# Kernel optimization log

Measured on AMD Instinct MI355X. Metric: run time of the kernel, lower is better.

Reference implementation:

```python
import jax, jax.numpy as jnp
import numpy as np

B, T, D, K = 64, 4096, 90, 32
LOG2PI = 1.8378770664093453


def setup_inputs() -> dict:
    key = jax.random.key(0)
    k1, k2, k3, k4, k5 = jax.random.split(key, 5)
    X = jax.random.normal(k1, (B, T, D), dtype=jnp.float32)
    state_priors = jax.random.uniform(k2, (K,), dtype=jnp.float32)
    transition_matrix = jax.random.uniform(k3, (K, K), dtype=jnp.float32)
    mu = jax.random.normal(k4, (K, D), dtype=jnp.float32) * 0.5
    log_var = jax.random.normal(k5, (K, D), dtype=jnp.float32) * 0.1
    return {"X": X, "state_priors": state_priors,
            "transition_matrix": transition_matrix, "mu": mu, "log_var": log_var}


def _emission_logprobs(X, mu, log_var):
    # Diagonal-Gaussian log density per state: (B,T,K)
    # expand (x-mu)^2*inv_var to avoid materializing a (B,T,K,D) tensor
    inv_var = jnp.exp(-log_var)                                   # (K,D)
    quad = (jnp.einsum('btd,kd->btk', X * X, inv_var)
            - 2.0 * jnp.einsum('btd,kd->btk', X, mu * inv_var)
            + jnp.sum(mu * mu * inv_var, axis=-1))                # (B,T,K)
    return -0.5 * (quad + jnp.sum(log_var, axis=-1) + D * LOG2PI)


def reference(X, state_priors, transition_matrix, mu, log_var):
    log_A = jax.nn.log_softmax(transition_matrix, axis=1)   # (K,K)
    log_pi = jax.nn.log_softmax(state_priors, axis=0)       # (K,)
    em = _emission_logprobs(X, mu, log_var)                 # (B,T,K)

    log_alpha0 = log_pi + em[:, 0, :]                       # (B,K)

    def step(log_alpha, e_t):
        # log_alpha: (B,K), e_t: (B,K)
        la = e_t + jax.nn.logsumexp(log_alpha[:, :, None] + log_A[None], axis=1)
        return la, None

    em_rest = jnp.swapaxes(em[:, 1:, :], 0, 1)              # (T-1,B,K)
    log_alpha_T, _ = jax.lax.scan(step, log_alpha0, em_rest)
    # sum over subjects of logsumexp over states at final timestep
    return jnp.sum(jax.nn.logsumexp(log_alpha_T, axis=-1))
```

## Files before the change

### kernel.cpp

```cpp
#include <hip/hip_runtime.h>
#include <stdint.h>

#define B_ 64
#define T_ 4096
#define D_ 90
#define K_ 32
#define CH_ 32
#define F_  128

typedef float f32x16 __attribute__((ext_vector_type(16)));
typedef __bf16 bf16x8 __attribute__((ext_vector_type(8)));

#define WS_A     0
#define WS_PI    1024
#define WS_C0    1056
#define WS_WF    1088
#define WS_EACC  4160
#define WS_MS    12352
#define WS_E     20544
#define WS_Q     4214848

__device__ __forceinline__ int perm_r(int r) {
  int t2 = (r >> 2) & 3;
  return r + ((t2 == 1) ? 4 : (t2 == 2) ? -4 : 0);
}
__device__ __forceinline__ uint32_t pk2(float hi, float lo) {
  return __builtin_amdgcn_perm(__float_as_uint(hi), __float_as_uint(lo), 0x07060302u);
}
__device__ __forceinline__ uint32_t rnd_pk(float hi, float lo) {
  uint32_t uh = __float_as_uint(hi) + 0x8000u;
  uint32_t ul = __float_as_uint(lo) + 0x8000u;
  return __builtin_amdgcn_perm(uh, ul, 0x07060302u);
}
__device__ __forceinline__ float bf2f(ushort u) {
  return __uint_as_float(((uint32_t)u) << 16);
}
__device__ __forceinline__ bf16x8 mkbf(uint32_t a, uint32_t b, uint32_t c, uint32_t d) {
  union { uint32_t u[4]; bf16x8 v; } x;
  x.u[0] = a; x.u[1] = b; x.u[2] = c; x.u[3] = d;
  return x.v;
}

__global__ __launch_bounds__(1024) void prep_kernel(
    const float* __restrict__ priors, const float* __restrict__ trans,
    const float* __restrict__ mu, const float* __restrict__ lv,
    float* __restrict__ ws) {
  int tid = threadIdx.x;
  {
    float v = trans[tid];
    float m = v;
    #pragma unroll
    for (int mk = 16; mk; mk >>= 1) m = fmaxf(m, __shfl_xor(m, mk));
    float e = expf(v - m);
    float s = e;
    #pragma unroll
    for (int mk = 16; mk; mk >>= 1) s += __shfl_xor(s, mk);
    ws[WS_A + tid] = e / s;
  }
  if (tid < 32) {
    float v = priors[tid];
    float m = v;
    #pragma unroll
    for (int mk = 16; mk; mk >>= 1) m = fmaxf(m, __shfl_xor(m, mk));
    float e = expf(v - m);
    float s = e;
    #pragma unroll
    for (int mk = 16; mk; mk >>= 1) s += __shfl_xor(s, mk);
    ws[WS_PI + tid] = e / s;
  }
  for (int i = tid; i < 6144; i += 1024) {
    int j = i & 7, l = (i >> 3) & 63, cm = i >> 9;
    int c = cm >> 1, mat = cm & 1;
    int h = l >> 5, nn = l & 31;
    int d = 16 * c + 8 * h + j;
    float v = 0.0f;
    if (d < D_) {
      float ivd = expf(-lv[nn * D_ + d]);
      v = (mat == 0) ? -0.5f * ivd : mu[nn * D_ + d] * ivd;
    }
    ((ushort*)(ws + WS_WF))[i] = (ushort)((__float_as_uint(v) + 0x8000u) >> 16);
  }
  if (tid < 32) {
    float s = 0.0f;
    for (int d = 0; d < D_; ++d) {
      float l  = lv[tid * D_ + d];
      float iv = expf(-l);
      float m_ = mu[tid * D_ + d];
      s += m_ * m_ * iv + l;
    }
    ws[WS_C0 + tid] = -0.5f * (s + (float)D_ * 1.8378770664093453f);
  }
}

__global__ __launch_bounds__(256) void emis_kernel(const float* __restrict__ X,
                                                   float* __restrict__ ws) {
  __shared__ float xs[4 * 2888];
  int tid = threadIdx.x;
  int l = tid & 63;
  int w = tid >> 6;
  int n = l & 31, h = l >> 5;
  int tB = blockIdx.x << 7;
  const float4* Xg = (const float4*)(X + (size_t)tB * D_);
  #pragma unroll
  for (int it = 0; it < 12; ++it) {
    int i = tid + (it << 8);
    if (i < 2880) {
      int g = i / 720;
      ((float4*)xs)[g * 722 + (i - g * 720)] = Xg[i];
    }
  }
  const uint4* wfp = (const uint4*)((const ushort*)(ws + WS_WF));
  uint4 wf[12];
  #pragma unroll
  for (int cm = 0; cm < 12; ++cm) wf[cm] = wfp[cm * 64 + l];
  float c0 = ws[WS_C0 + n];
  __syncthreads();
  int t0 = tB + (w << 5);
  int b  = t0 >> 12;
  const float* xrow = xs + w * 2888 + n * 90;
  f32x16 acc1, acc2;
  #pragma unroll
  for (int r = 0; r < 16; ++r) { acc1[r] = 0.0f; acc2[r] = 0.0f; }
  #pragma unroll
  for (int c = 0; c < 6; ++c) {
    float x[8];
    int s = 16 * c + 8 * h;
    const float2* p = (const float2*)(xrow + s);
    #pragma unroll
    for (int r = 0; r < 4; ++r) { float2 v = p[r]; x[2*r] = v.x; x[2*r+1] = v.y; }
    if (c == 5) {
      #pragma unroll
      for (int j = 0; j < 8; ++j) if (s + j >= D_) x[j] = 0.0f;
    }
    union { uint32_t u[4]; bf16x8 v; } xb, x2b;
    #pragma unroll
    for (int r = 0; r < 4; ++r) {
      xb.u[r]  = rnd_pk(x[2*r+1], x[2*r]);
      x2b.u[r] = rnd_pk(x[2*r+1] * x[2*r+1], x[2*r] * x[2*r]);
    }
    union { uint4 u; bf16x8 v; } w2, w1;
    w2.u = wf[c * 2]; w1.u = wf[c * 2 + 1];
    acc1 = __builtin_amdgcn_mfma_f32_32x32x16_bf16(xb.v,  w1.v, acc1, 0, 0, 0);
    acc2 = __builtin_amdgcn_mfma_f32_32x32x16_bf16(x2b.v, w2.v, acc2, 0, 0, 0);
  }
  float em[16], mrow[16];
  #pragma unroll
  for (int r = 0; r < 16; ++r) {
    float v = acc1[r] + acc2[r] + c0;
    em[r] = v;
    float m = v;
    #pragma unroll
    for (int mk = 1; mk <= 16; mk <<= 1) m = fmaxf(m, __shfl_xor(m, mk));
    mrow[r] = m;
  }
  ushort* Ew = (ushort*)(ws + WS_E);
  size_t ebase = (size_t)(b * K_ + n) * T_ + (t0 & (T_ - 1));
  #pragma unroll
  for (int q = 0; q < 4; ++q) {
    float e0 = exp2f((em[4*q]   - mrow[4*q])   * 1.44269504088896f);
    float e1 = exp2f((em[4*q+1] - mrow[4*q+1]) * 1.44269504088896f);
    float e2 = exp2f((em[4*q+2] - mrow[4*q+2]) * 1.44269504088896f);
    float e3 = exp2f((em[4*q+3] - mrow[4*q+3]) * 1.44269504088896f);
    uint2 d;
    d.x = rnd_pk(e1, e0);
    d.y = rnd_pk(e3, e2);
    *(uint2*)(Ew + ebase + 8 * q + 4 * h) = d;
  }
  float msum = 0.0f;
  #pragma unroll
  for (int r = 0; r < 16; ++r) msum += mrow[r];
  msum += __shfl_xor(msum, 32);
  if (l == 0) ws[WS_MS + (t0 >> 5)] = msum;
}

__global__ __launch_bounds__(128) void chunk_kernel(float* __restrict__ ws) {
  int l = threadIdx.x & 63;
  int h = l >> 5, n = l & 31;
  int bc = (blockIdx.x << 1) | (threadIdx.x >> 6);
  int b = bc >> 7, c = bc & (F_ - 1);
  int col = perm_r(n);
  const float* A = ws + WS_A;
  float astat[16];
  #pragma unroll
  for (int j = 0; j < 8; ++j) {
    astat[j]     = A[(8 * h + j) * K_ + col];
    astat[8 + j] = A[(16 + 8 * h + j) * K_ + col];
  }
  uint32_t q[8];
  #pragma unroll
  for (int r = 0; r < 4; ++r) {
    int s0 = 8 * h + 2 * r;
    uint32_t lo = (s0 == n)     ? 0x3F80u : 0u;
    uint32_t hi = (s0 + 1 == n) ? 0x3F80u : 0u;
    q[r] = lo | (hi << 16);
    int s2 = s0 + 16;
    lo = (s2 == n)     ? 0x3F80u : 0u;
    hi = (s2 + 1 == n) ? 0x3F80u : 0u;
    q[4 + r] = lo | (hi << 16);
  }
  const ushort* Eb = (const ushort*)(ws + WS_E) + (size_t)(b * K_ + col) * T_ + c * CH_;
  int eacc = 0;
  const f32x16 z = {0.f,0.f,0.f,0.f,0.f,0.f,0.f,0.f,0.f,0.f,0.f,0.f,0.f,0.f,0.f,0.f};
  f32x16 acc;
  #pragma unroll
  for (int r = 0; r < 16; ++r) acc[r] = 0.0f;

  auto step = [&](float e0) {
    uint32_t au[8];
    #pragma unroll
    for (int r = 0; r < 4; ++r) {
      au[r]     = pk2(astat[2 * r + 1] * e0, astat[2 * r] * e0);
      au[4 + r] = pk2(astat[8 + 2 * r + 1] * e0, astat[8 + 2 * r] * e0);
    }
    bf16x8 alo = mkbf(au[0], au[1], au[2], au[3]);
    bf16x8 ahi = mkbf(au[4], au[5], au[6], au[7]);
    bf16x8 qlo = mkbf(q[0], q[1], q[2], q[3]);
    bf16x8 qhi = mkbf(q[4], q[5], q[6], q[7]);
    acc = __builtin_amdgcn_mfma_f32_32x32x16_bf16(alo, qlo, z, 0, 0, 0);
    acc = __builtin_amdgcn_mfma_f32_32x32x16_bf16(ahi, qhi, acc, 0, 0, 0);
    #pragma unroll
    for (int r = 0; r < 4; ++r) {
      q[r]     = pk2(acc[2 * r + 1], acc[2 * r]);
      q[4 + r] = pk2(acc[8 + 2 * r + 1], acc[8 + 2 * r]);
    }
  };
  auto renorm = [&]() {
    float m = acc[0];
    #pragma unroll
    for (int r = 1; r < 16; ++r) m = fmaxf(m, acc[r]);
    #pragma unroll
    for (int mk = 1; mk <= 32; mk <<= 1) m = fmaxf(m, __shfl_xor(m, mk));
    int ex;
    frexpf(m, &ex);
    float sc = ldexpf(1.0f, -ex);
    eacc += ex;
    #pragma unroll
    for (int r = 0; r < 16; ++r) acc[r] *= sc;
    #pragma unroll
    for (int r = 0; r < 4; ++r) {
      q[r]     = pk2(acc[2 * r + 1], acc[2 * r]);
      q[4 + r] = pk2(acc[8 + 2 * r + 1], acc[8 + 2 * r]);
    }
  };

  uint4 ev = *(const uint4*)(Eb);
  int gstart = 0;
  if (c == 0) {
    uint4 evn = *(const uint4*)(Eb + 8);
    #pragma unroll
    for (int j = 1; j < 8; ++j) {
      uint32_t u = ((const uint32_t*)&ev)[j >> 1];
      step(bf2f((j & 1) ? (ushort)(u >> 16) : (ushort)(u & 0xFFFF)));
    }
    renorm();
    ev = evn;
    gstart = 1;
  }
  for (int g = gstart; g < CH_ / 8; ++g) {
    uint4 evn;
    if (g < CH_ / 8 - 1) evn = *(const uint4*)(Eb + 8 * (g + 1));
    #pragma unroll
    for (int j = 0; j < 8; ++j) {
      uint32_t u = ((const uint32_t*)&ev)[j >> 1];
      step(bf2f((j & 1) ? (ushort)(u >> 16) : (ushort)(u & 0xFFFF)));
    }
    renorm();
    ev = evn;
  }
  float* Qout = ws + WS_Q + (size_t)bc * (K_ * K_);
  #pragma unroll
  for (int r = 0; r < 16; ++r) {
    int m_ = (r & 3) + 8 * (r >> 2) + 4 * h;
    Qout[perm_r(m_) * K_ + n] = acc[r];
  }
  if (l == 0) ((int*)ws)[WS_EACC + bc] = eacc;
}

__global__ __launch_bounds__(512) void combine_kernel(float* __restrict__ ws,
                                                      float* __restrict__ out) {
  __shared__ float pm[8][32 * 34];
  __shared__ int   pe[8];
  int tid = threadIdx.x;
  int l = tid & 63, w = tid >> 6;
  int h = l >> 5, n = l & 31;
  int b = blockIdx.x;
  int row = perm_r(n);
  const float* Qb = ws + WS_Q + (size_t)b * (F_ * K_ * K_);
  const ushort* Ew = (const ushort*)(ws + WS_E);
  float alpha0 = 0.0f, msm = 0.0f;
  if (w == 0) {
    alpha0 = ws[WS_PI + n] * bf2f(Ew[(size_t)(b * K_ + n) * T_]);
    msm = ws[WS_MS + b * 128 + l] + ws[WS_MS + b * 128 + 64 + l];
  }
  int eacc = 0;
  {
    const int* ea = ((const int*)ws) + WS_EACC + b * F_ + w * 16;
    int v = (l < 16) ? ea[l] : 0;
    #pragma unroll
    for (int mk = 1; mk <= 8; mk <<= 1) v += __shfl_xor(v, mk);
    eacc = __shfl(v, 0);
  }
  uint32_t q[8];
  #pragma unroll
  for (int r = 0; r < 4; ++r) {
    int s0 = 8 * h + 2 * r;
    uint32_t lo = (s0 == n)     ? 0x3F80u : 0u;
    uint32_t hi = (s0 + 1 == n) ? 0x3F80u : 0u;
    q[r] = lo | (hi << 16);
    int s2 = s0 + 16;
    lo = (s2 == n)     ? 0x3F80u : 0u;
    hi = (s2 + 1 == n) ? 0x3F80u : 0u;
    q[4 + r] = lo | (hi << 16);
  }
  f32x16 acc;
  #pragma unroll
  for (int r = 0; r < 16; ++r) acc[r] = 0.0f;
  const f32x16 z = {0.f,0.f,0.f,0.f,0.f,0.f,0.f,0.f,0.f,0.f,0.f,0.f,0.f,0.f,0.f,0.f};

  auto lmul = [&](const float* a) {
    uint32_t au[8];
    #pragma unroll
    for (int r = 0; r < 4; ++r) {
      au[r]     = pk2(a[2 * r + 1], a[2 * r]);
      au[4 + r] = pk2(a[8 + 2 * r + 1], a[8 + 2 * r]);
    }
    bf16x8 alo = mkbf(au[0], au[1], au[2], au[3]);
    bf16x8 ahi = mkbf(au[4], au[5], au[6], au[7]);
    bf16x8 qlo = mkbf(q[0], q[1], q[2], q[3]);
    bf16x8 qhi = mkbf(q[4], q[5], q[6], q[7]);
    acc = __builtin_amdgcn_mfma_f32_32x32x16_bf16(alo, qlo, z, 0, 0, 0);
    acc = __builtin_amdgcn_mfma_f32_32x32x16_bf16(ahi, qhi, acc, 0, 0, 0);
    #pragma unroll
    for (int r = 0; r < 4; ++r) {
      q[r]     = pk2(acc[2 * r + 1], acc[2 * r]);
      q[4 + r] = pk2(acc[8 + 2 * r + 1], acc[8 + 2 * r]);
    }
  };
  auto renorm = [&]() {
    float m = acc[0];
    #pragma unroll
    for (int r = 1; r < 16; ++r) m = fmaxf(m, acc[r]);
    #pragma unroll
    for (int mk = 1; mk <= 32; mk <<= 1) m = fmaxf(m, __shfl_xor(m, mk));
    int ex;
    frexpf(m, &ex);
    float sc = ldexpf(1.0f, -ex);
    eacc += ex;
    #pragma unroll
    for (int r = 0; r < 16; ++r) acc[r] *= sc;
    #pragma unroll
    for (int r = 0; r < 4; ++r) {
      q[r]     = pk2(acc[2 * r + 1], acc[2 * r]);
      q[4 + r] = pk2(acc[8 + 2 * r + 1], acc[8 + 2 * r]);
    }
  };

  float4 ring[4][4];
  #pragma unroll
  for (int p = 0; p < 4; ++p) {
    const float* Mc = Qb + (size_t)(w * 16 + p) * 1024 + row * 32;
    ring[p][0] = *(const float4*)(Mc + 8 * h);
    ring[p][1] = *(const float4*)(Mc + 8 * h + 4);
    ring[p][2] = *(const float4*)(Mc + 16 + 8 * h);
    ring[p][3] = *(const float4*)(Mc + 16 + 8 * h + 4);
  }
  #pragma unroll
  for (int c = 0; c < 16; ++c) {
    float a[16];
    #pragma unroll
    for (int j = 0; j < 16; ++j) a[j] = ((const float*)&ring[c & 3][0])[j];
    lmul(a);
    if (c + 4 < 16) {
      const float* Mc = Qb + (size_t)(w * 16 + c + 4) * 1024 + row * 32;
      ring[c & 3][0] = *(const float4*)(Mc + 8 * h);
      ring[c & 3][1] = *(const float4*)(Mc + 8 * h + 4);
      ring[c & 3][2] = *(const float4*)(Mc + 16 + 8 * h);
      ring[c & 3][3] = *(const float4*)(Mc + 16 + 8 * h + 4);
    }
    if ((c & 3) == 3) renorm();
  }
  #pragma unroll
  for (int r = 0; r < 16; ++r) {
    int m_ = (r & 3) + 8 * (r >> 2) + 4 * h;
    pm[w][perm_r(m_) * 34 + n] = acc[r];
  }
  if (l == 0) pe[w] = eacc;
  __syncthreads();

  if (w == 0) {
    #pragma unroll
    for (int r = 0; r < 4; ++r) {
      int s0 = 8 * h + 2 * r;
      uint32_t lo = (s0 == n)     ? 0x3F80u : 0u;
      uint32_t hi = (s0 + 1 == n) ? 0x3F80u : 0u;
      q[r] = lo | (hi << 16);
      int s2 = s0 + 16;
      lo = (s2 == n)     ? 0x3F80u : 0u;
      hi = (s2 + 1 == n) ? 0x3F80u : 0u;
      q[4 + r] = lo | (hi << 16);
    }
    #pragma unroll
    for (int p = 0; p < 8; ++p) {
      float a[16];
      const float* base = &pm[p][row * 34];
      #pragma unroll
      for (int j = 0; j < 8; ++j) {
        a[j]     = base[8 * h + j];
        a[8 + j] = base[16 + 8 * h + j];
      }
      lmul(a);
    }
    int et = (l < 8) ? pe[l] : 0;
    #pragma unroll
    for (int mk = 1; mk <= 4; mk <<= 1) et += __shfl_xor(et, mk);
    et = __shfl(et, 0);
    float part = 0.0f;
    #pragma unroll
    for (int r = 0; r < 16; ++r) part += acc[r];
    part *= alpha0;
    #pragma unroll
    for (int mk = 1; mk <= 32; mk <<= 1) part += __shfl_xor(part, mk);
    #pragma unroll
    for (int mk = 32; mk; mk >>= 1) msm += __shfl_xor(msm, mk);
    if (l == 0) {
      float res = logf(part) + (float)et * 0.69314718055994531f + msm;
      atomicAdd(out, res);
    }
  }
}

extern "C" void kernel_launch(void* const* d_in, const int* in_sizes, int n_in,
                              void* d_out, int out_size, void* d_ws, size_t ws_size,
                              hipStream_t stream) {
  (void)in_sizes; (void)n_in; (void)out_size; (void)ws_size;
  const float* X      = (const float*)d_in[0];
  const float* priors = (const float*)d_in[1];
  const float* trans  = (const float*)d_in[2];
  const float* mu     = (const float*)d_in[3];
  const float* lv     = (const float*)d_in[4];
  float* ws  = (float*)d_ws;
  float* out = (float*)d_out;
  hipMemsetAsync(out, 0, sizeof(float), stream);
  prep_kernel<<<1, 1024, 0, stream>>>(priors, trans, mu, lv, ws);
  emis_kernel<<<2048, 256, 0, stream>>>(X, ws);
  chunk_kernel<<<B_ * F_ / 2, 128, 0, stream>>>(ws);
  combine_kernel<<<B_, 512, 0, stream>>>(ws, out);
}
```

Measured before the change: 211.5 us.

## Fuse emission and chunk-product kernels, keep emissions in LDS, split combine

Merges the emission kernel and the per-chunk transition-product kernel into one kernel, so bf16 emission values stay in shared memory and no longer round-trip through a large global buffer. X is converted to bf16 while being staged into LDS. Chunk products and partial combine matrices are stored as bf16 instead of fp32. The combine step is split into two kernels so the first stage runs across more blocks. This removes global traffic and a launch, but adds extra bf16 truncation of the intermediate matrices and one more small launch.

```diff
diff --git a/kernel.cpp b/kernel.cpp
--- a/kernel.cpp
+++ b/kernel.cpp
@@ -17,8 +17,10 @@
 #define WS_WF    1088
 #define WS_EACC  4160
 #define WS_MS    12352
-#define WS_E     20544
-#define WS_Q     4214848
+#define WS_E0    20544
+#define WS_PE    21568
+#define WS_PM    22080
+#define WS_Q     284224
 
 __device__ __forceinline__ int perm_r(int r) {
   int t2 = (r >> 2) & 3;
@@ -92,12 +94,12 @@
   }
 }
 
-__global__ __launch_bounds__(256) void emis_kernel(const float* __restrict__ X,
-                                                   float* __restrict__ ws) {
-  __shared__ float xs[4 * 2888];
+__global__ __launch_bounds__(256, 3) void fused_kernel(const float* __restrict__ X,
+                                                       float* __restrict__ ws) {
+  __shared__ ushort xsb[4][32 * 104];
+  __shared__ ushort els[4][32 * 40];
   int tid = threadIdx.x;
-  int l = tid & 63;
-  int w = tid >> 6;
+  int l = tid & 63, w = tid >> 6;
   int n = l & 31, h = l >> 5;
   int tB = blockIdx.x << 7;
   const float4* Xg = (const float4*)(X + (size_t)tB * D_);
@@ -105,9 +107,21 @@
   for (int it = 0; it < 12; ++it) {
     int i = tid + (it << 8);
     if (i < 2880) {
+      float4 v = Xg[i];
       int g = i / 720;
-      ((float4*)xs)[g * 722 + (i - g * 720)] = Xg[i];
-    }
+      int f = (i - g * 720) * 4;
+      uint32_t d0 = rnd_pk(v.y, v.x);
+      uint32_t d1 = rnd_pk(v.w, v.z);
+      int r0 = f / 90;        int c0_ = f - r0 * 90;
+      int r1 = (f + 2) / 90;  int c1_ = (f + 2) - r1 * 90;
+      *(uint32_t*)&xsb[g][r0 * 104 + c0_] = d0;
+      *(uint32_t*)&xsb[g][r1 * 104 + c1_] = d1;
+    }
+  }
+  for (int i = tid; i < 896; i += 256) {
+    int r = i / 7;
+    int d = 90 + 2 * (i - r * 7);
+    *(uint32_t*)&xsb[r >> 5][(r & 31) * 104 + d] = 0u;
   }
   const uint4* wfp = (const uint4*)((const ushort*)(ws + WS_WF));
   uint4 wf[12];
@@ -115,29 +129,28 @@
   for (int cm = 0; cm < 12; ++cm) wf[cm] = wfp[cm * 64 + l];
   float c0 = ws[WS_C0 + n];
   __syncthreads();
+
   int t0 = tB + (w << 5);
   int b  = t0 >> 12;
-  const float* xrow = xs + w * 2888 + n * 90;
+  int bc = t0 >> 5;
+  const ushort* xrow = &xsb[w][n * 104];
   f32x16 acc1, acc2;
   #pragma unroll
   for (int r = 0; r < 16; ++r) { acc1[r] = 0.0f; acc2[r] = 0.0f; }
   #pragma unroll
   for (int c = 0; c < 6; ++c) {
+    union { uint4 u; bf16x8 v; } xb;
+    xb.u = *(const uint4*)(xrow + 16 * c + 8 * h);
     float x[8];
-    int s = 16 * c + 8 * h;
-    const float2* p = (const float2*)(xrow + s);
-    #pragma unroll
-    for (int r = 0; r < 4; ++r) { float2 v = p[r]; x[2*r] = v.x; x[2*r+1] = v.y; }
-    if (c == 5) {
-      #pragma unroll
-      for (int j = 0; j < 8; ++j) if (s + j >= D_) x[j] = 0.0f;
-    }
-    union { uint32_t u[4]; bf16x8 v; } xb, x2b;
-    #pragma unroll
-    for (int r = 0; r < 4; ++r) {
-      xb.u[r]  = rnd_pk(x[2*r+1], x[2*r]);
+    #pragma unroll
+    for (int j = 0; j < 8; ++j) {
+      uint32_t uu = ((const uint32_t*)&xb.u)[j >> 1];
+      x[j] = bf2f((j & 1) ? (ushort)(uu >> 16) : (ushort)(uu & 0xFFFF));
+    }
+    union { uint32_t u[4]; bf16x8 v; } x2b;
+    #pragma unroll
+    for (int r = 0; r < 4; ++r)
       x2b.u[r] = rnd_pk(x[2*r+1] * x[2*r+1], x[2*r] * x[2*r]);
-    }
     union { uint4 u; bf16x8 v; } w2, w1;
     w2.u = wf[c * 2]; w1.u = wf[c * 2 + 1];
     acc1 = __builtin_amdgcn_mfma_f32_32x32x16_bf16(xb.v,  w1.v, acc1, 0, 0, 0);
@@ -153,8 +166,7 @@
     for (int mk = 1; mk <= 16; mk <<= 1) m = fmaxf(m, __shfl_xor(m, mk));
     mrow[r] = m;
   }
-  ushort* Ew = (ushort*)(ws + WS_E);
-  size_t ebase = (size_t)(b * K_ + n) * T_ + (t0 & (T_ - 1));
+  ushort* Ew = els[w];
   #pragma unroll
   for (int q = 0; q < 4; ++q) {
     float e0 = exp2f((em[4*q]   - mrow[4*q])   * 1.44269504088896f);
@@ -164,20 +176,17 @@
     uint2 d;
     d.x = rnd_pk(e1, e0);
     d.y = rnd_pk(e3, e2);
-    *(uint2*)(Ew + ebase + 8 * q + 4 * h) = d;
+    *(uint2*)(Ew + n * 40 + 8 * q + 4 * h) = d;
+    if (q == 0 && h == 0 && (t0 & (T_ - 1)) == 0)
+      ((ushort*)(ws + WS_E0))[b * K_ + n] = (ushort)(d.x & 0xFFFF);
   }
   float msum = 0.0f;
   #pragma unroll
   for (int r = 0; r < 16; ++r) msum += mrow[r];
   msum += __shfl_xor(msum, 32);
-  if (l == 0) ws[WS_MS + (t0 >> 5)] = msum;
-}
-
-__global__ __launch_bounds__(128) void chunk_kernel(float* __restrict__ ws) {
-  int l = threadIdx.x & 63;
-  int h = l >> 5, n = l & 31;
-  int bc = (blockIdx.x << 1) | (threadIdx.x >> 6);
-  int b = bc >> 7, c = bc & (F_ - 1);
+  if (l == 0) ws[WS_MS + bc] = msum;
+  __syncthreads();
+
   int col = perm_r(n);
   const float* A = ws + WS_A;
   float astat[16];
@@ -198,7 +207,6 @@
     hi = (s2 + 1 == n) ? 0x3F80u : 0u;
     q[4 + r] = lo | (hi << 16);
   }
-  const ushort* Eb = (const ushort*)(ws + WS_E) + (size_t)(b * K_ + col) * T_ + c * CH_;
   int eacc = 0;
   const f32x16 z = {0.f,0.f,0.f,0.f,0.f,0.f,0.f,0.f,0.f,0.f,0.f,0.f,0.f,0.f,0.f,0.f};
   f32x16 acc;
@@ -243,56 +251,44 @@
     }
   };
 
-  uint4 ev = *(const uint4*)(Eb);
-  int gstart = 0;
-  if (c == 0) {
-    uint4 evn = *(const uint4*)(Eb + 8);
+  const ushort* Eb = els[w] + col * 40;
+  int g0 = 0;
+  if ((t0 & (T_ - 1)) == 0) {
+    uint4 ev = *(const uint4*)(Eb);
     #pragma unroll
     for (int j = 1; j < 8; ++j) {
       uint32_t u = ((const uint32_t*)&ev)[j >> 1];
       step(bf2f((j & 1) ? (ushort)(u >> 16) : (ushort)(u & 0xFFFF)));
     }
     renorm();
-    ev = evn;
-    gstart = 1;
-  }
-  for (int g = gstart; g < CH_ / 8; ++g) {
-    uint4 evn;
-    if (g < CH_ / 8 - 1) evn = *(const uint4*)(Eb + 8 * (g + 1));
+    g0 = 1;
+  }
+  for (int g = g0; g < CH_ / 8; ++g) {
+    uint4 ev = *(const uint4*)(Eb + 8 * g);
     #pragma unroll
     for (int j = 0; j < 8; ++j) {
       uint32_t u = ((const uint32_t*)&ev)[j >> 1];
       step(bf2f((j & 1) ? (ushort)(u >> 16) : (ushort)(u & 0xFFFF)));
     }
     renorm();
-    ev = evn;
-  }
-  float* Qout = ws + WS_Q + (size_t)bc * (K_ * K_);
+  }
+  ushort* Qo = (ushort*)(ws + WS_Q) + (size_t)bc * (K_ * K_);
   #pragma unroll
   for (int r = 0; r < 16; ++r) {
     int m_ = (r & 3) + 8 * (r >> 2) + 4 * h;
-    Qout[perm_r(m_) * K_ + n] = acc[r];
+    Qo[perm_r(m_) * K_ + n] = (ushort)(__float_as_uint(acc[r]) >> 16);
   }
   if (l == 0) ((int*)ws)[WS_EACC + bc] = eacc;
 }
 
-__global__ __launch_bounds__(512) void combine_kernel(float* __restrict__ ws,
-                                                      float* __restrict__ out) {
-  __shared__ float pm[8][32 * 34];
-  __shared__ int   pe[8];
-  int tid = threadIdx.x;
-  int l = tid & 63, w = tid >> 6;
+__global__ __launch_bounds__(64) void combine1_kernel(float* __restrict__ ws) {
+  int l = threadIdx.x;
   int h = l >> 5, n = l & 31;
-  int b = blockIdx.x;
+  int bw = blockIdx.x;
+  int b = bw >> 3, w = bw & 7;
   int row = perm_r(n);
-  const float* Qb = ws + WS_Q + (size_t)b * (F_ * K_ * K_);
-  const ushort* Ew = (const ushort*)(ws + WS_E);
-  float alpha0 = 0.0f, msm = 0.0f;
-  if (w == 0) {
-    alpha0 = ws[WS_PI + n] * bf2f(Ew[(size_t)(b * K_ + n) * T_]);
-    msm = ws[WS_MS + b * 128 + l] + ws[WS_MS + b * 128 + 64 + l];
-  }
-  int eacc = 0;
+  const ushort* Qb = (const ushort*)(ws + WS_Q) + (size_t)(b * F_ + w * 16) * (K_ * K_);
+  int eacc;
   {
     const int* ea = ((const int*)ws) + WS_EACC + b * F_ + w * 16;
     int v = (l < 16) ? ea[l] : 0;
@@ -317,15 +313,9 @@
   for (int r = 0; r < 16; ++r) acc[r] = 0.0f;
   const f32x16 z = {0.f,0.f,0.f,0.f,0.f,0.f,0.f,0.f,0.f,0.f,0.f,0.f,0.f,0.f,0.f,0.f};
 
-  auto lmul = [&](const float* a) {
-    uint32_t au[8];
-    #pragma unroll
-    for (int r = 0; r < 4; ++r) {
-      au[r]     = pk2(a[2 * r + 1], a[2 * r]);
-      au[4 + r] = pk2(a[8 + 2 * r + 1], a[8 + 2 * r]);
-    }
-    bf16x8 alo = mkbf(au[0], au[1], au[2], au[3]);
-    bf16x8 ahi = mkbf(au[4], au[5], au[6], au[7]);
+  auto lmul = [&](uint4 lo, uint4 hi) {
+    bf16x8 alo = mkbf(lo.x, lo.y, lo.z, lo.w);
+    bf16x8 ahi = mkbf(hi.x, hi.y, hi.z, hi.w);
     bf16x8 qlo = mkbf(q[0], q[1], q[2], q[3]);
     bf16x8 qhi = mkbf(q[4], q[5], q[6], q[7]);
     acc = __builtin_amdgcn_mfma_f32_32x32x16_bf16(alo, qlo, z, 0, 0, 0);
@@ -355,77 +345,89 @@
     }
   };
 
-  float4 ring[4][4];
+  uint4 rlo[4], rhi[4];
   #pragma unroll
   for (int p = 0; p < 4; ++p) {
-    const float* Mc = Qb + (size_t)(w * 16 + p) * 1024 + row * 32;
-    ring[p][0] = *(const float4*)(Mc + 8 * h);
-    ring[p][1] = *(const float4*)(Mc + 8 * h + 4);
-    ring[p][2] = *(const float4*)(Mc + 16 + 8 * h);
-    ring[p][3] = *(const float4*)(Mc + 16 + 8 * h + 4);
+    const ushort* Mc = Qb + (size_t)p * (K_ * K_) + row * K_;
+    rlo[p] = *(const uint4*)(Mc + 8 * h);
+    rhi[p] = *(const uint4*)(Mc + 16 + 8 * h);
   }
   #pragma unroll
   for (int c = 0; c < 16; ++c) {
-    float a[16];
-    #pragma unroll
-    for (int j = 0; j < 16; ++j) a[j] = ((const float*)&ring[c & 3][0])[j];
-    lmul(a);
+    lmul(rlo[c & 3], rhi[c & 3]);
     if (c + 4 < 16) {
-      const float* Mc = Qb + (size_t)(w * 16 + c + 4) * 1024 + row * 32;
-      ring[c & 3][0] = *(const float4*)(Mc + 8 * h);
-      ring[c & 3][1] = *(const float4*)(Mc + 8 * h + 4);
-      ring[c & 3][2] = *(const float4*)(Mc + 16 + 8 * h);
-      ring[c & 3][3] = *(const float4*)(Mc + 16 + 8 * h + 4);
+      const ushort* Mc = Qb + (size_t)(c + 4) * (K_ * K_) + row * K_;
+      rlo[c & 3] = *(const uint4*)(Mc + 8 * h);
+      rhi[c & 3] = *(const uint4*)(Mc + 16 + 8 * h);
     }
     if ((c & 3) == 3) renorm();
   }
+  ushort* pmq = (ushort*)(ws + WS_PM) + (size_t)bw * (K_ * K_);
   #pragma unroll
   for (int r = 0; r < 16; ++r) {
     int m_ = (r & 3) + 8 * (r >> 2) + 4 * h;
-    pm[w][perm_r(m_) * 34 + n] = acc[r];
-  }
-  if (l == 0) pe[w] = eacc;
-  __syncthreads();
-
-  if (w == 0) {
-    #pragma unroll
-    for (int r = 0; r < 4; ++r) {
-      int s0 = 8 * h + 2 * r;
-      uint32_t lo = (s0 == n)     ? 0x3F80u : 0u;
-      uint32_t hi = (s0 + 1 == n) ? 0x3F80u : 0u;
-      q[r] = lo | (hi << 16);
-      int s2 = s0 + 16;
-      lo = (s2 == n)     ? 0x3F80u : 0u;
-      hi = (s2 + 1 == n) ? 0x3F80u : 0u;
-      q[4 + r] = lo | (hi << 16);
-    }
-    #pragma unroll
-    for (int p = 0; p < 8; ++p) {
-      float a[16];
-      const float* base = &pm[p][row * 34];
-      #pragma unroll
-      for (int j = 0; j < 8; ++j) {
-        a[j]     = base[8 * h + j];
-        a[8 + j] = base[16 + 8 * h + j];
-      }
-      lmul(a);
-    }
-    int et = (l < 8) ? pe[l] : 0;
-    #pragma unroll
-    for (int mk = 1; mk <= 4; mk <<= 1) et += __shfl_xor(et, mk);
-    et = __shfl(et, 0);
-    float part = 0.0f;
-    #pragma unroll
-    for (int r = 0; r < 16; ++r) part += acc[r];
-    part *= alpha0;
-    #pragma unroll
-    for (int mk = 1; mk <= 32; mk <<= 1) part += __shfl_xor(part, mk);
-    #pragma unroll
-    for (int mk = 32; mk; mk >>= 1) msm += __shfl_xor(msm, mk);
-    if (l == 0) {
-      float res = logf(part) + (float)et * 0.69314718055994531f + msm;
-      atomicAdd(out, res);
-    }
+    pmq[perm_r(m_) * K_ + n] = (ushort)(__float_as_uint(acc[r]) >> 16);
+  }
+  if (l == 0) ((int*)ws)[WS_PE + bw] = eacc;
+}
+
+__global__ __launch_bounds__(64) void combine2_kernel(float* __restrict__ ws,
+                                                      float* __restrict__ out) {
+  int l = threadIdx.x;
+  int h = l >> 5, n = l & 31;
+  int b = blockIdx.x;
+  int row = perm_r(n);
+  float alpha0 = ws[WS_PI + n] * bf2f(((const ushort*)(ws + WS_E0))[b * K_ + n]);
+  float msm = ws[WS_MS + b * 128 + l] + ws[WS_MS + b * 128 + 64 + l];
+  uint32_t q[8];
+  #pragma unroll
+  for (int r = 0; r < 4; ++r) {
+    int s0 = 8 * h + 2 * r;
+    uint32_t lo = (s0 == n)     ? 0x3F80u : 0u;
+    uint32_t hi = (s0 + 1 == n) ? 0x3F80u : 0u;
+    q[r] = lo | (hi << 16);
+    int s2 = s0 + 16;
+    lo = (s2 == n)     ? 0x3F80u : 0u;
+    hi = (s2 + 1 == n) ? 0x3F80u : 0u;
+    q[4 + r] = lo | (hi << 16);
+  }
+  f32x16 acc;
+  #pragma unroll
+  for (int r = 0; r < 16; ++r) acc[r] = 0.0f;
+  const f32x16 z = {0.f,0.f,0.f,0.f,0.f,0.f,0.f,0.f,0.f,0.f,0.f,0.f,0.f,0.f,0.f,0.f};
+  const ushort* pmq = (const ushort*)(ws + WS_PM) + (size_t)b * 8 * (K_ * K_);
+  #pragma unroll
+  for (int p = 0; p < 8; ++p) {
+    const ushort* base = pmq + p * (K_ * K_) + row * K_;
+    uint4 lo = *(const uint4*)(base + 8 * h);
+    uint4 hi = *(const uint4*)(base + 16 + 8 * h);
+    bf16x8 alo = mkbf(lo.x, lo.y, lo.z, lo.w);
+    bf16x8 ahi = mkbf(hi.x, hi.y, hi.z, hi.w);
+    bf16x8 qlo = mkbf(q[0], q[1], q[2], q[3]);
+    bf16x8 qhi = mkbf(q[4], q[5], q[6], q[7]);
+    acc = __builtin_amdgcn_mfma_f32_32x32x16_bf16(alo, qlo, z, 0, 0, 0);
+    acc = __builtin_amdgcn_mfma_f32_32x32x16_bf16(ahi, qhi, acc, 0, 0, 0);
+    #pragma unroll
+    for (int r = 0; r < 4; ++r) {
+      q[r]     = pk2(acc[2 * r + 1], acc[2 * r]);
+      q[4 + r] = pk2(acc[8 + 2 * r + 1], acc[8 + 2 * r]);
+    }
+  }
+  int et = (l < 8) ? ((const int*)ws)[WS_PE + b * 8 + l] : 0;
+  #pragma unroll
+  for (int mk = 1; mk <= 4; mk <<= 1) et += __shfl_xor(et, mk);
+  et = __shfl(et, 0);
+  float part = 0.0f;
+  #pragma unroll
+  for (int r = 0; r < 16; ++r) part += acc[r];
+  part *= alpha0;
+  #pragma unroll
+  for (int mk = 1; mk <= 32; mk <<= 1) part += __shfl_xor(part, mk);
+  #pragma unroll
+  for (int mk = 32; mk; mk >>= 1) msm += __shfl_xor(msm, mk);
+  if (l == 0) {
+    float res = logf(part) + (float)et * 0.69314718055994531f + msm;
+    atomicAdd(out, res);
   }
 }
 
@@ -442,7 +444,7 @@
   float* out = (float*)d_out;
   hipMemsetAsync(out, 0, sizeof(float), stream);
   prep_kernel<<<1, 1024, 0, stream>>>(priors, trans, mu, lv, ws);
-  emis_kernel<<<2048, 256, 0, stream>>>(X, ws);
-  chunk_kernel<<<B_ * F_ / 2, 128, 0, stream>>>(ws);
-  combine_kernel<<<B_, 512, 0, stream>>>(ws, out);
-}
+  fused_kernel<<<B_ * T_ / 128, 256, 0, stream>>>(X, ws);
+  combine1_kernel<<<B_ * 8, 64, 0, stream>>>(ws);
+  combine2_kernel<<<B_, 64, 0, stream>>>(ws, out);
+}
```

After: 187.8 us. -11.2%, faster.
